# Kernel tuning notes

Measured on AMD Instinct MI355X. Metric: run time of the kernel, lower is better.

Reference implementation:

```python
import jax, jax.numpy as jnp
import numpy as np

LAYERS = [1024, 2048, 1024]
OPTIONS = 4
BATCH = 2048


def setup_inputs() -> dict:
    key = jax.random.key(0)
    k_x, k_idx, k_w1, k_w2 = jax.random.split(key, 4)
    x = jax.random.normal(k_x, (BATCH, LAYERS[0]), dtype=jnp.float32)
    idx = jax.random.randint(k_idx, (BATCH,), 0, OPTIONS, dtype=jnp.int64)
    # xavier-normal-ish scaled weights per layer: shape [options, in, out]
    std1 = float(np.sqrt(2.0 / (LAYERS[0] * LAYERS[1] + OPTIONS * LAYERS[1])))
    std2 = float(np.sqrt(2.0 / (LAYERS[1] * LAYERS[2] + OPTIONS * LAYERS[2])))
    W1 = jax.random.normal(k_w1, (OPTIONS, LAYERS[0], LAYERS[1]), dtype=jnp.float32) * std1
    b1 = jnp.zeros((OPTIONS, LAYERS[1]), dtype=jnp.float32)
    W2 = jax.random.normal(k_w2, (OPTIONS, LAYERS[1], LAYERS[2]), dtype=jnp.float32) * std2
    b2 = jnp.zeros((OPTIONS, LAYERS[2]), dtype=jnp.float32)
    return {"x": x, "idx": idx, "W1": W1, "b1": b1, "W2": W2, "b2": b2}


def reference(x, idx, W1, b1, W2, b2):
    # Original: torch.bmm(x[:,None,:], W[idx]) + b[zeros_like(idx)]
    # Equivalent math without materializing the [B, in, out] gathered weights:
    # compute all options densely, then select per-sample option with idx.
    # NOTE: bias is ALWAYS option 0 (faithful to the original's zeros_like(idx)).
    def layer(h, W, b):
        h_all = jnp.einsum('bi,oij->boj', h, W)  # [B, O, out]
        h_sel = jnp.take_along_axis(h_all, idx[:, None, None], axis=1)[:, 0, :]  # [B, out]
        return h_sel + b[0][None, :]

    h = layer(x, W1, b1)
    out = layer(h, W2, b2)
    return out
```

## Files before the change

### kernel.cpp

```cpp
#include <hip/hip_runtime.h>
#include <stdint.h>

typedef __bf16 bf16x8 __attribute__((ext_vector_type(8)));
typedef float f32x4 __attribute__((ext_vector_type(4)));
typedef unsigned short u16;
typedef const __attribute__((address_space(1))) void* as1_cvp;
typedef __attribute__((address_space(3))) void* as3_vp;

__device__ __forceinline__ u16 f2bf(float f) {
  union { float f; unsigned u; } v; v.f = f;
  unsigned r = v.u + 0x7fffu + ((v.u >> 16) & 1u);
  return (u16)(r >> 16);
}

__global__ __launch_bounds__(256) void hist_perm_kernel(
    const int* __restrict__ idx, int n, int* __restrict__ starts,
    int* __restrict__ perm, int* __restrict__ tmap) {
  __shared__ int cnt[4][256];
  __shared__ int gtot[4], gstart[4];
  const int t = threadIdx.x;
  const int rpt = (n + 255) >> 8;
  const int base = t * rpt;
  int c[4] = {0, 0, 0, 0};
  for (int j = 0; j < rpt; ++j) {
    const int i = base + j;
    if (i < n) c[idx[i] & 3]++;
  }
  #pragma unroll
  for (int g = 0; g < 4; ++g) cnt[g][t] = c[g];
  __syncthreads();

  const int w = t >> 6, l = t & 63;
  {
    const int s0 = cnt[w][l * 4 + 0], s1 = cnt[w][l * 4 + 1];
    const int s2 = cnt[w][l * 4 + 2], s3 = cnt[w][l * 4 + 3];
    const int sum = s0 + s1 + s2 + s3;
    int sc = sum;
    #pragma unroll
    for (int d = 1; d < 64; d <<= 1) {
      const int o = __shfl_up(sc, d, 64);
      if (l >= d) sc += o;
    }
    const int ex = sc - sum;
    cnt[w][l * 4 + 0] = ex;
    cnt[w][l * 4 + 1] = ex + s0;
    cnt[w][l * 4 + 2] = ex + s0 + s1;
    cnt[w][l * 4 + 3] = ex + s0 + s1 + s2;
    if (l == 63) gtot[w] = sc;
  }
  __syncthreads();

  if (t == 0) {
    int s = 0, nt = 0;
    for (int g = 0; g < 4; ++g) {
      gstart[g] = s;
      starts[g] = s;
      const int cg = gtot[g];
      for (int j = 0; j < cg; j += 128) tmap[nt++] = (g << 28) | (s + j);
      s += cg;
    }
    starts[4] = s;
    while (nt < 20) tmap[nt++] = -1;
  }
  __syncthreads();

  int run[4] = {0, 0, 0, 0};
  for (int j = 0; j < rpt; ++j) {
    const int i = base + j;
    if (i < n) {
      const int g = idx[i] & 3;
      perm[gstart[g] + cnt[g][t] + run[g]] = i;
      run[g]++;
    }
  }
}

__global__ __launch_bounds__(256) void gather_convert(
    const float* __restrict__ x, const int* __restrict__ perm,
    u16* __restrict__ Xs) {
  const int p = blockIdx.x;
  const int b = perm[p];
  const float4 v = ((const float4*)(x + (size_t)b * 1024))[threadIdx.x];
  ushort4 u;
  u.x = f2bf(v.x); u.y = f2bf(v.y); u.z = f2bf(v.z); u.w = f2bf(v.w);
  ((ushort4*)(Xs + (size_t)p * 1024))[threadIdx.x] = u;
}

__global__ __launch_bounds__(256) void transpose_both(
    const float* __restrict__ W1, u16* __restrict__ W1T,
    const float* __restrict__ W2, u16* __restrict__ W2T) {
  __shared__ float tile[64][65];
  int bid = blockIdx.x;
  const float* W; u16* WT; int K, N, tx, ty, o;
  if (bid < 2048) {
    W = W1; WT = W1T; K = 1024; N = 2048;
    o = bid >> 9; const int t = bid & 511; tx = t & 31; ty = t >> 5;
  } else {
    bid -= 2048;
    W = W2; WT = W2T; K = 2048; N = 1024;
    o = bid >> 9; const int t = bid & 511; tx = t & 15; ty = t >> 4;
  }
  const float* Wo = W + (size_t)o * K * N;
  u16* WTo = WT + (size_t)o * N * K;
  const int k0 = ty * 64, n0 = tx * 64;
  const int rr = threadIdx.x >> 4, cc = threadIdx.x & 15;
  #pragma unroll
  for (int j = 0; j < 4; ++j) {
    const int r = j * 16 + rr;
    const float4 v = *(const float4*)(Wo + (size_t)(k0 + r) * N + n0 + cc * 4);
    tile[r][cc * 4 + 0] = v.x; tile[r][cc * 4 + 1] = v.y;
    tile[r][cc * 4 + 2] = v.z; tile[r][cc * 4 + 3] = v.w;
  }
  __syncthreads();
  #pragma unroll
  for (int j = 0; j < 4; ++j) {
    const int nrow = j * 16 + rr;
    ushort4 u;
    u.x = f2bf(tile[cc * 4 + 0][nrow]);
    u.y = f2bf(tile[cc * 4 + 1][nrow]);
    u.z = f2bf(tile[cc * 4 + 2][nrow]);
    u.w = f2bf(tile[cc * 4 + 3][nrow]);
    *(ushort4*)(WTo + (size_t)(n0 + nrow) * K + k0 + cc * 4) = u;
  }
}

template <int EPI, int KT, int NN, int S, int NTN>
__global__ __launch_bounds__(256, 2) void gemm_kernel(
    const u16* __restrict__ A, const u16* __restrict__ BT,
    const float* __restrict__ bias, const int* __restrict__ starts,
    const int* __restrict__ tmap, u16* __restrict__ outH,
    float* __restrict__ outP, int batchB) {
  __shared__ char smem[65536];

  constexpr int NT_PAD = 20;
  const int nwg = NT_PAD * NTN * S;
  const int q = nwg >> 3;
  const int bid = blockIdx.x;
  const int swz = (bid & 7) * q + (bid >> 3);
  const int tile = swz % NT_PAD;
  const int n_t = (swz / NT_PAD) % NTN;
  const int s = swz / (NT_PAD * NTN);

  const int tm = tmap[tile];
  if (tm < 0) return;
  const int o = tm >> 28;
  const int m_start = tm & 0x0FFFFFFF;
  const int g1 = starts[o + 1];
  const int n_start = n_t * 128;
  const int kb0 = s * (KT / S);
  const u16* Bo = BT + (size_t)o * NN * KT;

  const int tid = threadIdx.x;
  const int w = tid >> 6;
  const int l = tid & 63;
  const int wm = w >> 1, wn = w & 1;
  const int l8 = l & 7, ld8 = l >> 3;

  const int src_unit = l8 ^ (ld8 & 7);

  const u16* pA[4];
  #pragma unroll
  for (int j = 0; j < 4; ++j) {
    int r = m_start + (j * 4 + w) * 8 + ld8;
    if (r >= g1) r = g1 - 1;
    pA[j] = A + (size_t)r * KT + kb0 + src_unit * 8;
  }
  const u16* pB[4];
  #pragma unroll
  for (int j = 0; j < 4; ++j) {
    const int nr = n_start + (j * 4 + w) * 8 + ld8;
    pB[j] = Bo + (size_t)nr * KT + kb0 + src_unit * 8;
  }

#define STAGE(dst_off)                                                         \
  {                                                                            \
    _Pragma("unroll")                                                          \
    for (int j = 0; j < 4; ++j)                                                \
      __builtin_amdgcn_global_load_lds((as1_cvp)pA[j],                         \
          (as3_vp)(smem + (dst_off) + (j * 4 + w) * 1024), 16, 0, 0);          \
    _Pragma("unroll")                                                          \
    for (int j = 0; j < 4; ++j)                                                \
      __builtin_amdgcn_global_load_lds((as1_cvp)pB[j],                         \
          (as3_vp)(smem + (dst_off) + 16384 + (j * 4 + w) * 1024), 16, 0, 0);  \
    _Pragma("unroll") for (int j = 0; j < 4; ++j) pA[j] += 64;                 \
    _Pragma("unroll") for (int j = 0; j < 4; ++j) pB[j] += 64;                 \
  }

  const int lrow = l & 15;
  const int lx = l & 7;
  const int lu = l >> 4;
  int offA[4][2], offB[4][2];
  #pragma unroll
  for (int a = 0; a < 4; ++a)
    #pragma unroll
    for (int kk = 0; kk < 2; ++kk)
      offA[a][kk] = (wm * 64 + a * 16 + lrow) * 128 + (((kk * 4 + lu) ^ lx) << 4);
  #pragma unroll
  for (int b = 0; b < 4; ++b)
    #pragma unroll
    for (int kk = 0; kk < 2; ++kk)
      offB[b][kk] = (wn * 64 + b * 16 + lrow) * 128 + (((kk * 4 + lu) ^ lx) << 4);

  f32x4 acc[4][4] = {};

  const int nK = (KT / S) >> 6;
  STAGE(0);
  for (int kt = 0; kt < nK; ++kt) {
    const int cur = (kt & 1) << 15;
    if (kt + 1 < nK) {
      STAGE(cur ^ 32768);
      asm volatile("s_waitcnt vmcnt(8)" ::: "memory");
    } else {
      asm volatile("s_waitcnt vmcnt(0)" ::: "memory");
    }
    __builtin_amdgcn_s_barrier();

    bf16x8 af[4][2], bfr[4][2];
    #pragma unroll
    for (int a = 0; a < 4; ++a)
      #pragma unroll
      for (int kk = 0; kk < 2; ++kk)
        af[a][kk] = *(const bf16x8*)(smem + cur + offA[a][kk]);
    #pragma unroll
    for (int b = 0; b < 4; ++b)
      #pragma unroll
      for (int kk = 0; kk < 2; ++kk)
        bfr[b][kk] = *(const bf16x8*)(smem + cur + 16384 + offB[b][kk]);
    asm volatile("s_waitcnt lgkmcnt(0)" ::: "memory");
    __builtin_amdgcn_s_barrier();

    __builtin_amdgcn_s_setprio(1);
    #pragma unroll
    for (int kk = 0; kk < 2; ++kk)
      #pragma unroll
      for (int a = 0; a < 4; ++a)
        #pragma unroll
        for (int b = 0; b < 4; ++b)
          acc[a][b] = __builtin_amdgcn_mfma_f32_16x16x32_bf16(af[a][kk], bfr[b][kk], acc[a][b], 0, 0, 0);
    __builtin_amdgcn_s_setprio(0);
  }
#undef STAGE

  const int col_l = l & 15;
  const int row_l = (l >> 4) << 2;
  #pragma unroll
  for (int a = 0; a < 4; ++a) {
    #pragma unroll
    for (int b = 0; b < 4; ++b) {
      const int n = n_start + wn * 64 + b * 16 + col_l;
      float bv = 0.f;
      if (EPI == 0) bv = bias[n];
      #pragma unroll
      for (int r = 0; r < 4; ++r) {
        const int p = m_start + wm * 64 + a * 16 + row_l + r;
        if (p < g1) {
          if (EPI == 0) {
            outH[(size_t)p * NN + n] = f2bf(acc[a][b][r] + bv);
          } else {
            outP[((size_t)(s * batchB + p)) * NN + n] = acc[a][b][r];
          }
        }
      }
    }
  }
}

__global__ __launch_bounds__(256) void reduce_kernel(
    const float* __restrict__ part, const float* __restrict__ b2,
    const int* __restrict__ perm, float* __restrict__ out, int batchB) {
  const int p = blockIdx.x;
  const int t = threadIdx.x;
  const float4 v0 = ((const float4*)(part + (size_t)p * 1024))[t];
  const float4 v1 = ((const float4*)(part + (size_t)(batchB + p) * 1024))[t];
  const float4 bv = ((const float4*)b2)[t];
  float4 r;
  r.x = v0.x + v1.x + bv.x;
  r.y = v0.y + v1.y + bv.y;
  r.z = v0.z + v1.z + bv.z;
  r.w = v0.w + v1.w + bv.w;
  ((float4*)(out + (size_t)perm[p] * 1024))[t] = r;
}

extern "C" void kernel_launch(void* const* d_in, const int* in_sizes, int n_in,
                              void* d_out, int out_size, void* d_ws, size_t ws_size,
                              hipStream_t stream) {
  (void)n_in; (void)out_size; (void)ws_size;
  const float* x   = (const float*)d_in[0];
  const int*   idx = (const int*)d_in[1];
  const float* W1  = (const float*)d_in[2];
  const float* b1  = (const float*)d_in[3];
  const float* W2  = (const float*)d_in[4];
  const float* b2  = (const float*)d_in[5];
  float* out = (float*)d_out;

  const int B = in_sizes[1];

  char* ws = (char*)d_ws;
  u16* W1T     = (u16*)(ws);
  float* part  = (float*)(ws);
  u16* W2T     = (u16*)(ws + 16777216);
  u16* Xs      = (u16*)(ws + 33554432);
  u16* Hs      = (u16*)(ws + 37748736);
  int* perm    = (int*)(ws + 46137344);
  int* starts  = (int*)(ws + 46137344 + 8192);
  int* tmap    = starts + 64;

  hist_perm_kernel<<<1, 256, 0, stream>>>(idx, B, starts, perm, tmap);
  transpose_both<<<4096, 256, 0, stream>>>(W1, W1T, W2, W2T);
  gather_convert<<<B, 256, 0, stream>>>(x, perm, Xs);

  gemm_kernel<0, 1024, 2048, 1, 16><<<320, 256, 0, stream>>>(
      Xs, W1T, b1, starts, tmap, Hs, nullptr, B);
  gemm_kernel<1, 2048, 1024, 2, 8><<<320, 256, 0, stream>>>(
      Hs, W2T, nullptr, starts, tmap, nullptr, part, B);
  reduce_kernel<<<B, 256, 0, stream>>>(part, b2, perm, out, B);
}
```

Before: 78.31 us.

## Replace split-K second GEMM with 64-row tiles writing output directly

Replaces the split-K=2 second GEMM and its separate reduce kernel with full-K tiles of 64 rows. This keeps the same workgroup count, adds the bias and scatters the result through perm straight into the output. The gather/convert kernel is also merged into the weight-transpose launch, and the histogram kernel emits tile maps for both 128- and 64-row tiles. The goal is to drop the fp32 partial buffer round-trip and two launches. The cost is a smaller M tile that reuses B less, and scattered output rows.

```diff
diff --git a/kernel.cpp b/kernel.cpp
--- a/kernel.cpp
+++ b/kernel.cpp
@@ -15,7 +15,8 @@
 
 __global__ __launch_bounds__(256) void hist_perm_kernel(
     const int* __restrict__ idx, int n, int* __restrict__ starts,
-    int* __restrict__ perm, int* __restrict__ tmap) {
+    int* __restrict__ perm, int* __restrict__ tmap128,
+    int* __restrict__ tmap64) {
   __shared__ int cnt[4][256];
   __shared__ int gtot[4], gstart[4];
   const int t = threadIdx.x;
@@ -51,16 +52,18 @@
   __syncthreads();
 
   if (t == 0) {
-    int s = 0, nt = 0;
+    int s = 0, nt128 = 0, nt64 = 0;
     for (int g = 0; g < 4; ++g) {
       gstart[g] = s;
       starts[g] = s;
       const int cg = gtot[g];
-      for (int j = 0; j < cg; j += 128) tmap[nt++] = (g << 28) | (s + j);
+      for (int j = 0; j < cg; j += 128) tmap128[nt128++] = (g << 28) | (s + j);
+      for (int j = 0; j < cg; j += 64)  tmap64[nt64++]  = (g << 28) | (s + j);
       s += cg;
     }
     starts[4] = s;
-    while (nt < 20) tmap[nt++] = -1;
+    while (nt128 < 20) tmap128[nt128++] = -1;
+    while (nt64 < 40)  tmap64[nt64++]  = -1;
   }
   __syncthreads();
 
@@ -75,22 +78,22 @@
   }
 }
 
-__global__ __launch_bounds__(256) void gather_convert(
+__global__ __launch_bounds__(256) void prep_kernel(
+    const float* __restrict__ W1, u16* __restrict__ W1T,
+    const float* __restrict__ W2, u16* __restrict__ W2T,
     const float* __restrict__ x, const int* __restrict__ perm,
     u16* __restrict__ Xs) {
-  const int p = blockIdx.x;
-  const int b = perm[p];
-  const float4 v = ((const float4*)(x + (size_t)b * 1024))[threadIdx.x];
-  ushort4 u;
-  u.x = f2bf(v.x); u.y = f2bf(v.y); u.z = f2bf(v.z); u.w = f2bf(v.w);
-  ((ushort4*)(Xs + (size_t)p * 1024))[threadIdx.x] = u;
-}
-
-__global__ __launch_bounds__(256) void transpose_both(
-    const float* __restrict__ W1, u16* __restrict__ W1T,
-    const float* __restrict__ W2, u16* __restrict__ W2T) {
   __shared__ float tile[64][65];
   int bid = blockIdx.x;
+  if (bid >= 4096) {
+    const int p = bid - 4096;
+    const int b = perm[p];
+    const float4 v = ((const float4*)(x + (size_t)b * 1024))[threadIdx.x];
+    ushort4 u;
+    u.x = f2bf(v.x); u.y = f2bf(v.y); u.z = f2bf(v.z); u.w = f2bf(v.w);
+    ((ushort4*)(Xs + (size_t)p * 1024))[threadIdx.x] = u;
+    return;
+  }
   const float* W; u16* WT; int K, N, tx, ty, o;
   if (bid < 2048) {
     W = W1; WT = W1T; K = 1024; N = 2048;
@@ -124,22 +127,23 @@
   }
 }
 
-template <int EPI, int KT, int NN, int S, int NTN>
+template <int EPI, int TM, int NT_PAD, int KT, int NN, int NTN>
 __global__ __launch_bounds__(256, 2) void gemm_kernel(
     const u16* __restrict__ A, const u16* __restrict__ BT,
     const float* __restrict__ bias, const int* __restrict__ starts,
-    const int* __restrict__ tmap, u16* __restrict__ outH,
-    float* __restrict__ outP, int batchB) {
-  __shared__ char smem[65536];
-
-  constexpr int NT_PAD = 20;
-  const int nwg = NT_PAD * NTN * S;
+    const int* __restrict__ tmap, const int* __restrict__ perm,
+    u16* __restrict__ outH, float* __restrict__ outF) {
+  constexpr int MR = TM / 32;
+  constexpr int ABUF = TM * 128;
+  constexpr int BSTR = ABUF + 16384;
+  __shared__ char smem[2 * BSTR];
+
+  const int nwg = NT_PAD * NTN;
   const int q = nwg >> 3;
   const int bid = blockIdx.x;
   const int swz = (bid & 7) * q + (bid >> 3);
   const int tile = swz % NT_PAD;
-  const int n_t = (swz / NT_PAD) % NTN;
-  const int s = swz / (NT_PAD * NTN);
+  const int n_t = swz / NT_PAD;
 
   const int tm = tmap[tile];
   if (tm < 0) return;
@@ -147,7 +151,6 @@
   const int m_start = tm & 0x0FFFFFFF;
   const int g1 = starts[o + 1];
   const int n_start = n_t * 128;
-  const int kb0 = s * (KT / S);
   const u16* Bo = BT + (size_t)o * NN * KT;
 
   const int tid = threadIdx.x;
@@ -158,66 +161,69 @@
 
   const int src_unit = l8 ^ (ld8 & 7);
 
-  const u16* pA[4];
-  #pragma unroll
-  for (int j = 0; j < 4; ++j) {
+  const u16* pA[MR];
+  #pragma unroll
+  for (int j = 0; j < MR; ++j) {
     int r = m_start + (j * 4 + w) * 8 + ld8;
     if (r >= g1) r = g1 - 1;
-    pA[j] = A + (size_t)r * KT + kb0 + src_unit * 8;
+    pA[j] = A + (size_t)r * KT + src_unit * 8;
   }
   const u16* pB[4];
   #pragma unroll
   for (int j = 0; j < 4; ++j) {
     const int nr = n_start + (j * 4 + w) * 8 + ld8;
-    pB[j] = Bo + (size_t)nr * KT + kb0 + src_unit * 8;
+    pB[j] = Bo + (size_t)nr * KT + src_unit * 8;
   }
 
 #define STAGE(dst_off)                                                         \
   {                                                                            \
     _Pragma("unroll")                                                          \
-    for (int j = 0; j < 4; ++j)                                                \
+    for (int j = 0; j < MR; ++j)                                               \
       __builtin_amdgcn_global_load_lds((as1_cvp)pA[j],                         \
           (as3_vp)(smem + (dst_off) + (j * 4 + w) * 1024), 16, 0, 0);          \
     _Pragma("unroll")                                                          \
     for (int j = 0; j < 4; ++j)                                                \
       __builtin_amdgcn_global_load_lds((as1_cvp)pB[j],                         \
-          (as3_vp)(smem + (dst_off) + 16384 + (j * 4 + w) * 1024), 16, 0, 0);  \
-    _Pragma("unroll") for (int j = 0; j < 4; ++j) pA[j] += 64;                 \
+          (as3_vp)(smem + (dst_off) + ABUF + (j * 4 + w) * 1024), 16, 0, 0);   \
+    _Pragma("unroll") for (int j = 0; j < MR; ++j) pA[j] += 64;                \
     _Pragma("unroll") for (int j = 0; j < 4; ++j) pB[j] += 64;                 \
   }
 
   const int lrow = l & 15;
   const int lx = l & 7;
   const int lu = l >> 4;
-  int offA[4][2], offB[4][2];
-  #pragma unroll
-  for (int a = 0; a < 4; ++a)
+  int offA[MR][2], offB[4][2];
+  #pragma unroll
+  for (int a = 0; a < MR; ++a)
     #pragma unroll
     for (int kk = 0; kk < 2; ++kk)
-      offA[a][kk] = (wm * 64 + a * 16 + lrow) * 128 + (((kk * 4 + lu) ^ lx) << 4);
+      offA[a][kk] = (wm * (TM / 2) + a * 16 + lrow) * 128 + (((kk * 4 + lu) ^ lx) << 4);
   #pragma unroll
   for (int b = 0; b < 4; ++b)
     #pragma unroll
     for (int kk = 0; kk < 2; ++kk)
       offB[b][kk] = (wn * 64 + b * 16 + lrow) * 128 + (((kk * 4 + lu) ^ lx) << 4);
 
-  f32x4 acc[4][4] = {};
-
-  const int nK = (KT / S) >> 6;
+  f32x4 acc[MR][4] = {};
+
+  const int nK = KT >> 6;
   STAGE(0);
   for (int kt = 0; kt < nK; ++kt) {
-    const int cur = (kt & 1) << 15;
+    const int cur = (kt & 1) * BSTR;
     if (kt + 1 < nK) {
-      STAGE(cur ^ 32768);
-      asm volatile("s_waitcnt vmcnt(8)" ::: "memory");
+      STAGE(BSTR - cur);
+      if constexpr (TM == 128)
+        asm volatile("s_waitcnt vmcnt(8)" ::: "memory");
+      else
+        asm volatile("s_waitcnt vmcnt(6)" ::: "memory");
     } else {
       asm volatile("s_waitcnt vmcnt(0)" ::: "memory");
     }
     __builtin_amdgcn_s_barrier();
 
-    bf16x8 af[4][2], bfr[4][2];
-    #pragma unroll
-    for (int a = 0; a < 4; ++a)
+    bf16x8 af[MR][2], bfr[4][2];
+    #pragma unroll
+    for (int a = 0; a < MR; ++a)
       #pragma unroll
       for (int kk = 0; kk < 2; ++kk)
         af[a][kk] = *(const bf16x8*)(smem + cur + offA[a][kk]);
@@ -225,7 +231,7 @@
     for (int b = 0; b < 4; ++b)
       #pragma unroll
       for (int kk = 0; kk < 2; ++kk)
-        bfr[b][kk] = *(const bf16x8*)(smem + cur + 16384 + offB[b][kk]);
+        bfr[b][kk] = *(const bf16x8*)(smem + cur + ABUF + offB[b][kk]);
     asm volatile("s_waitcnt lgkmcnt(0)" ::: "memory");
     __builtin_amdgcn_s_barrier();
 
@@ -233,7 +239,7 @@
     #pragma unroll
     for (int kk = 0; kk < 2; ++kk)
       #pragma unroll
-      for (int a = 0; a < 4; ++a)
+      for (int a = 0; a < MR; ++a)
         #pragma unroll
         for (int b = 0; b < 4; ++b)
           acc[a][b] = __builtin_amdgcn_mfma_f32_16x16x32_bf16(af[a][kk], bfr[b][kk], acc[a][b], 0, 0, 0);
@@ -244,41 +250,24 @@
   const int col_l = l & 15;
   const int row_l = (l >> 4) << 2;
   #pragma unroll
-  for (int a = 0; a < 4; ++a) {
+  for (int a = 0; a < MR; ++a) {
     #pragma unroll
     for (int b = 0; b < 4; ++b) {
       const int n = n_start + wn * 64 + b * 16 + col_l;
-      float bv = 0.f;
-      if (EPI == 0) bv = bias[n];
+      const float bv = bias[n];
       #pragma unroll
       for (int r = 0; r < 4; ++r) {
-        const int p = m_start + wm * 64 + a * 16 + row_l + r;
+        const int p = m_start + wm * (TM / 2) + a * 16 + row_l + r;
         if (p < g1) {
           if (EPI == 0) {
             outH[(size_t)p * NN + n] = f2bf(acc[a][b][r] + bv);
           } else {
-            outP[((size_t)(s * batchB + p)) * NN + n] = acc[a][b][r];
+            outF[(size_t)perm[p] * NN + n] = acc[a][b][r] + bv;
           }
         }
       }
     }
   }
-}
-
-__global__ __launch_bounds__(256) void reduce_kernel(
-    const float* __restrict__ part, const float* __restrict__ b2,
-    const int* __restrict__ perm, float* __restrict__ out, int batchB) {
-  const int p = blockIdx.x;
-  const int t = threadIdx.x;
-  const float4 v0 = ((const float4*)(part + (size_t)p * 1024))[t];
-  const float4 v1 = ((const float4*)(part + (size_t)(batchB + p) * 1024))[t];
-  const float4 bv = ((const float4*)b2)[t];
-  float4 r;
-  r.x = v0.x + v1.x + bv.x;
-  r.y = v0.y + v1.y + bv.y;
-  r.z = v0.z + v1.z + bv.z;
-  r.w = v0.w + v1.w + bv.w;
-  ((float4*)(out + (size_t)perm[p] * 1024))[t] = r;
 }
 
 extern "C" void kernel_launch(void* const* d_in, const int* in_sizes, int n_in,
@@ -297,21 +286,19 @@
 
   char* ws = (char*)d_ws;
   u16* W1T     = (u16*)(ws);
-  float* part  = (float*)(ws);
   u16* W2T     = (u16*)(ws + 16777216);
   u16* Xs      = (u16*)(ws + 33554432);
   u16* Hs      = (u16*)(ws + 37748736);
   int* perm    = (int*)(ws + 46137344);
   int* starts  = (int*)(ws + 46137344 + 8192);
-  int* tmap    = starts + 64;
-
-  hist_perm_kernel<<<1, 256, 0, stream>>>(idx, B, starts, perm, tmap);
-  transpose_both<<<4096, 256, 0, stream>>>(W1, W1T, W2, W2T);
-  gather_convert<<<B, 256, 0, stream>>>(x, perm, Xs);
-
-  gemm_kernel<0, 1024, 2048, 1, 16><<<320, 256, 0, stream>>>(
-      Xs, W1T, b1, starts, tmap, Hs, nullptr, B);
-  gemm_kernel<1, 2048, 1024, 2, 8><<<320, 256, 0, stream>>>(
-      Hs, W2T, nullptr, starts, tmap, nullptr, part, B);
-  reduce_kernel<<<B, 256, 0, stream>>>(part, b2, perm, out, B);
-}
+  int* tmap128 = starts + 64;
+  int* tmap64  = starts + 128;
+
+  hist_perm_kernel<<<1, 256, 0, stream>>>(idx, B, starts, perm, tmap128, tmap64);
+  prep_kernel<<<4096 + B, 256, 0, stream>>>(W1, W1T, W2, W2T, x, perm, Xs);
+
+  gemm_kernel<0, 128, 20, 1024, 2048, 16><<<320, 256, 0, stream>>>(
+      Xs, W1T, b1, starts, tmap128, perm, Hs, nullptr);
+  gemm_kernel<1, 64, 40, 2048, 1024, 8><<<320, 256, 0, stream>>>(
+      Hs, W2T, b2, starts, tmap64, perm, nullptr, out);
+}
```

New measurement: 78.90 us. No clear change (+0.8%).
